# Kernel optimization log

Measured on AMD Instinct MI355X. Metric: run time of the kernel, lower is better.

Reference implementation:

```python
import jax, jax.numpy as jnp
import numpy as np

N_QUBITS = 4
N_LAYERS = 2
FS = 2          # filter_size
STRIDE = 1
DIM = 2 ** N_QUBITS  # 16

# mean over qubits of PauliZ eigenvalue per computational-basis state
_idx = np.arange(DIM)
_bits = np.stack([(_idx >> (N_QUBITS - 1 - q)) & 1 for q in range(N_QUBITS)], 0)  # [4,16]
Z_MEAN = jnp.asarray((1.0 - 2.0 * _bits).mean(0), dtype=jnp.float32)               # [16]


def ry_mat(t):
    c, s = jnp.cos(t / 2), jnp.sin(t / 2)
    m = jnp.stack([jnp.stack([c, -s], -1), jnp.stack([s, c], -1)], -2)
    return m.astype(jnp.complex64)


def rx_mat(t):
    c = jnp.cos(t / 2).astype(jnp.complex64)
    s = (jnp.sin(t / 2) * (-1j)).astype(jnp.complex64)
    return jnp.stack([jnp.stack([c, s], -1), jnp.stack([s, c], -1)], -2)


def rz_mat(t):
    e = jnp.exp((t / 2).astype(jnp.complex64) * (-1j))
    z = jnp.zeros_like(e)
    return jnp.stack([jnp.stack([e, z], -1), jnp.stack([z, jnp.conj(e)], -1)], -2)


def apply_1q(state, U, q):
    # state: [N,2,2,2,2] complex; U: [2,2] or batched [N,2,2]
    st = jnp.moveaxis(state, 1 + q, -1)
    if U.ndim == 3:
        st = jnp.einsum('nab,n...b->n...a', U, st)
    else:
        st = jnp.einsum('ab,n...b->n...a', U, st)
    return jnp.moveaxis(st, -1, 1 + q)


def apply_cnot(state, c, t):
    st = jnp.moveaxis(state, (1 + c, 1 + t), (-2, -1))
    st = jnp.stack([st[..., 0, :], st[..., 1, ::-1]], axis=-2)
    return jnp.moveaxis(st, (-2, -1), (1 + c, 1 + t))


def apply_cry(state, theta, c, t):
    U = ry_mat(theta)
    st = jnp.moveaxis(state, (1 + c, 1 + t), (-2, -1))
    bot = jnp.einsum('ab,n...b->n...a', U, st[..., 1, :])
    st = jnp.stack([st[..., 0, :], bot], axis=-2)
    return jnp.moveaxis(st, (-2, -1), (1 + c, 1 + t))


def _forward(x, weights):
    B, H, W, C = x.shape
    oh = (H - FS) // STRIDE + 1
    ow = (W - FS) // STRIDE + 1
    # extract all patches at once: [B, oh, ow, FS, FS, C]
    ri = (jnp.arange(oh) * STRIDE)[:, None, None, None] + jnp.arange(FS)[None, None, :, None]
    ci = (jnp.arange(ow) * STRIDE)[None, :, None, None] + jnp.arange(FS)[None, None, None, :]
    patches = x[:, ri, ci, :]
    pf = patches.reshape(B * oh * ow, FS * FS * C)
    # tf.nn.l2_normalize over the whole (flat) patch, eps=1e-12
    norm = pf * jax.lax.rsqrt(jnp.maximum(jnp.sum(pf * pf, -1, keepdims=True), 1e-12))
    ang = norm[:, :N_QUBITS]  # RY angles, [N,4]
    N = pf.shape[0]

    # |0000> encoded state, batched over all patches
    state = jnp.zeros((N, DIM), jnp.complex64).at[:, 0].set(1.0)
    state = state.reshape((N,) + (2,) * N_QUBITS)
    for q in range(N_QUBITS):
        state = apply_1q(state, ry_mat(ang[:, q]), q)
    for q in range(N_QUBITS - 1):
        state = apply_cnot(state, q, q + 1)

    outs = []
    for f in range(weights.shape[0]):
        w = weights[f]
        s = state
        for layer in range(N_LAYERS):
            base = layer * N_QUBITS * 3
            for q in range(N_QUBITS):
                p = base + q * 3
                s = apply_1q(s, rx_mat(w[p]), q)
                s = apply_1q(s, ry_mat(w[p + 1]), q)
                s = apply_1q(s, rz_mat(w[p + 2]), q)
            # CRY on even pairs, reusing weights[base + i] (as in the source)
            for q in range(0, N_QUBITS - 1, 2):
                s = apply_cry(s, w[base + q], q, q + 1)
        sf = s.reshape(N, DIM)
        probs = jnp.real(sf * jnp.conj(sf))           # [N,16]
        outs.append((probs @ Z_MEAN).reshape(B, oh, ow))  # mean of <Z_q>
    return jnp.stack(outs, -1)  # [B, oh, ow, n_filters]


def setup_inputs() -> dict:
    key = jax.random.key(0)
    k1, k2 = jax.random.split(key)
    x = jax.random.normal(k1, (8, 96, 96, 16), dtype=jnp.float32)
    # keras 'random_uniform' initializer default range
    weights = jax.random.uniform(k2, (8, 24), dtype=jnp.float32, minval=-0.05, maxval=0.05)
    return {"x": x, "weights": weights}


def reference(x, weights):
    return _forward(x, weights)
```

## Files before the change

### kernel.cpp

```cpp
#include <hip/hip_runtime.h>

namespace {
constexpr int DIM = 16;
constexpr int BATCH = 8;
constexpr int H = 96, W = 96, CH = 16;
constexpr int OH = 95, OW = 95;
constexpr int NF = 8, NW = 24;
constexpr int NPIX = BATCH * OH * OW;
constexpr int PSIBLK = (NPIX + 255) / 256;
constexpr int PSI_OFF = NF * 256;
constexpr int PPB = 128;
constexpr int ABLK = (NPIX + PPB - 1) / PPB;
}

__device__ __forceinline__ int permf(int i) {
  int j = i;
  if (j & 8) j ^= 4;
  if (j & 4) j ^= 2;
  if (j & 2) j ^= 1;
  return j;
}

__global__ __launch_bounds__(256)
void prep_kernel(const float* __restrict__ x, const float* __restrict__ wts,
                 float* __restrict__ ws) {
  const int tid = threadIdx.x;
  if (blockIdx.x == PSIBLK) {
    __shared__ float ur[NF * 256];
    __shared__ float ui[NF * 256];
    const int f = tid >> 4;
    const int col = tid & 15;
    if (tid < NF * DIM) {
      const float* w = wts + f * NW;
      float ar[DIM], ai[DIM];
#pragma unroll
      for (int i = 0; i < DIM; ++i) { ar[i] = (i == col) ? 1.f : 0.f; ai[i] = 0.f; }
#pragma unroll
      for (int layer = 0; layer < 2; ++layer) {
        const int wb = layer * 12;
#pragma unroll
        for (int q = 0; q < 4; ++q) {
          const int m = 8 >> q;
          float c, s;
          {
            __sincosf(w[wb + q * 3] * 0.5f, &s, &c);
#pragma unroll
            for (int i = 0; i < DIM; ++i) {
              if (i & m) continue;
              const int j = i | m;
              const float a0r = ar[i], a0i = ai[i], a1r = ar[j], a1i = ai[j];
              ar[i] = fmaf(c, a0r,  s * a1i);
              ai[i] = fmaf(c, a0i, -s * a1r);
              ar[j] = fmaf(c, a1r,  s * a0i);
              ai[j] = fmaf(c, a1i, -s * a0r);
            }
          }
          {
            __sincosf(w[wb + q * 3 + 1] * 0.5f, &s, &c);
#pragma unroll
            for (int i = 0; i < DIM; ++i) {
              if (i & m) continue;
              const int j = i | m;
              const float a0r = ar[i], a0i = ai[i], a1r = ar[j], a1i = ai[j];
              ar[i] = fmaf(c, a0r, -s * a1r);
              ai[i] = fmaf(c, a0i, -s * a1i);
              ar[j] = fmaf(s, a0r,  c * a1r);
              ai[j] = fmaf(s, a0i,  c * a1i);
            }
          }
          {
            __sincosf(w[wb + q * 3 + 2] * 0.5f, &s, &c);
#pragma unroll
            for (int i = 0; i < DIM; ++i) {
              const float r = ar[i], im = ai[i];
              if (i & m) { ar[i] = fmaf(c, r, -s * im); ai[i] = fmaf(c, im,  s * r); }
              else       { ar[i] = fmaf(c, r,  s * im); ai[i] = fmaf(c, im, -s * r); }
            }
          }
        }
        {
          float c, s;
          __sincosf(w[wb + 0] * 0.5f, &s, &c);
#pragma unroll
          for (int i = 0; i < DIM; ++i) {
            if (!(i & 8) || (i & 4)) continue;
            const int j = i | 4;
            const float a0r = ar[i], a0i = ai[i], a1r = ar[j], a1i = ai[j];
            ar[i] = fmaf(c, a0r, -s * a1r);
            ai[i] = fmaf(c, a0i, -s * a1i);
            ar[j] = fmaf(s, a0r,  c * a1r);
            ai[j] = fmaf(s, a0i,  c * a1i);
          }
        }
        {
          float c, s;
          __sincosf(w[wb + 2] * 0.5f, &s, &c);
#pragma unroll
          for (int i = 0; i < DIM; ++i) {
            if (!(i & 2) || (i & 1)) continue;
            const int j = i | 1;
            const float a0r = ar[i], a0i = ai[i], a1r = ar[j], a1i = ai[j];
            ar[i] = fmaf(c, a0r, -s * a1r);
            ai[i] = fmaf(c, a0i, -s * a1i);
            ar[j] = fmaf(s, a0r,  c * a1r);
            ai[j] = fmaf(s, a0i,  c * a1i);
          }
        }
      }
#pragma unroll
      for (int i = 0; i < DIM; ++i) {
        ur[f * 256 + col * 16 + i] = ar[i];
        ui[f * 256 + col * 16 + i] = ai[i];
      }
    }
    __syncthreads();
    if (tid < NF * DIM) {
      const int k = col;
      const int pk = permf(k);
      const float* cr = ur + f * 256;
      const float* ci = ui + f * 256;
      float* dst = ws + f * 256 + k * 16;
#pragma unroll
      for (int j = 0; j < DIM; ++j) {
        const int pj = permf(j);
        float acc = 0.f;
#pragma unroll
        for (int i = 0; i < DIM; ++i) {
          const float z = 1.f - 0.5f * (float)__popc(i);
          acc += z * (cr[pk * 16 + i] * cr[pj * 16 + i] +
                      ci[pk * 16 + i] * ci[pj * 16 + i]);
        }
        dst[j] = acc;
      }
    }
  } else {
    const int n = blockIdx.x * 256 + tid;
    if (n >= NPIX) return;
    const int b = n / (OH * OW);
    const int rem = n - b * (OH * OW);
    const int oi = rem / OW;
    const int oj = rem - oi * OW;

    const float* base = x + (((b * H) + oi) * W + oj) * CH;
    float ss = 0.f;
    float4 f0 = make_float4(0.f, 0.f, 0.f, 0.f);
#pragma unroll
    for (int fi = 0; fi < 2; ++fi) {
      const float4* row = reinterpret_cast<const float4*>(base + fi * W * CH);
#pragma unroll
      for (int k = 0; k < 8; ++k) {
        const float4 v = row[k];
        if (fi == 0 && k == 0) f0 = v;
        ss = fmaf(v.x, v.x, ss); ss = fmaf(v.y, v.y, ss);
        ss = fmaf(v.z, v.z, ss); ss = fmaf(v.w, v.w, ss);
      }
    }
    const float inv = rsqrtf(fmaxf(ss, 1e-12f));

    float cq[4], sq[4];
    __sincosf(f0.x * inv * 0.5f, &sq[0], &cq[0]);
    __sincosf(f0.y * inv * 0.5f, &sq[1], &cq[1]);
    __sincosf(f0.z * inv * 0.5f, &sq[2], &cq[2]);
    __sincosf(f0.w * inv * 0.5f, &sq[3], &cq[3]);

    float st[DIM];
#pragma unroll
    for (int i = 0; i < DIM; ++i) {
      st[i] = ((i & 8) ? sq[0] : cq[0]) * ((i & 4) ? sq[1] : cq[1]) *
              ((i & 2) ? sq[2] : cq[2]) * ((i & 1) ? sq[3] : cq[3]);
    }
    float4* dst = reinterpret_cast<float4*>(ws + PSI_OFF + n * 16);
    dst[0] = make_float4(st[0], st[1], st[2], st[3]);
    dst[1] = make_float4(st[4], st[5], st[6], st[7]);
    dst[2] = make_float4(st[8], st[9], st[10], st[11]);
    dst[3] = make_float4(st[12], st[13], st[14], st[15]);
  }
}

__global__ __launch_bounds__(512)
void apply_kernel(const float* __restrict__ ws, float* __restrict__ out) {
  __shared__ float os[PPB * 9];
  const int tid = threadIdx.x;
  const int lane = tid & 63;
  const int f = __builtin_amdgcn_readfirstlane(tid >> 6);
  const float* __restrict__ M = ws + f * 256;
  const int pbase = blockIdx.x * PPB;

  const int n0 = pbase + lane;
  const int n1 = pbase + 64 + lane;
  const int c0 = n0 < NPIX ? n0 : NPIX - 1;
  const int c1 = n1 < NPIX ? n1 : NPIX - 1;

  float pa[DIM], pb[DIM];
  {
    const float4* p0 = reinterpret_cast<const float4*>(ws + PSI_OFF + c0 * 16);
    const float4 a0 = p0[0], a1 = p0[1], a2 = p0[2], a3 = p0[3];
    pa[0] = a0.x;  pa[1] = a0.y;  pa[2] = a0.z;  pa[3] = a0.w;
    pa[4] = a1.x;  pa[5] = a1.y;  pa[6] = a1.z;  pa[7] = a1.w;
    pa[8] = a2.x;  pa[9] = a2.y;  pa[10] = a2.z; pa[11] = a2.w;
    pa[12] = a3.x; pa[13] = a3.y; pa[14] = a3.z; pa[15] = a3.w;
    const float4* p1 = reinterpret_cast<const float4*>(ws + PSI_OFF + c1 * 16);
    const float4 b0 = p1[0], b1 = p1[1], b2 = p1[2], b3 = p1[3];
    pb[0] = b0.x;  pb[1] = b0.y;  pb[2] = b0.z;  pb[3] = b0.w;
    pb[4] = b1.x;  pb[5] = b1.y;  pb[6] = b1.z;  pb[7] = b1.w;
    pb[8] = b2.x;  pb[9] = b2.y;  pb[10] = b2.z; pb[11] = b2.w;
    pb[12] = b3.x; pb[13] = b3.y; pb[14] = b3.z; pb[15] = b3.w;
  }

  float ya[DIM], yb[DIM];
#pragma unroll
  for (int i = 0; i < DIM; ++i) { ya[i] = 0.f; yb[i] = 0.f; }

#pragma unroll
  for (int k = 0; k < DIM; ++k) {
    const float ak = pa[k];
    const float bk = pb[k];
#pragma unroll
    for (int j = 0; j < DIM; ++j) {
      const float m = M[k * 16 + j];
      ya[j] = fmaf(m, ak, ya[j]);
      yb[j] = fmaf(m, bk, yb[j]);
    }
  }

  float a0 = 0.f, a1 = 0.f, a2 = 0.f, a3 = 0.f;
  float b0 = 0.f, b1 = 0.f, b2 = 0.f, b3 = 0.f;
#pragma unroll
  for (int i = 0; i < DIM; i += 4) {
    a0 = fmaf(pa[i + 0], ya[i + 0], a0);
    a1 = fmaf(pa[i + 1], ya[i + 1], a1);
    a2 = fmaf(pa[i + 2], ya[i + 2], a2);
    a3 = fmaf(pa[i + 3], ya[i + 3], a3);
    b0 = fmaf(pb[i + 0], yb[i + 0], b0);
    b1 = fmaf(pb[i + 1], yb[i + 1], b1);
    b2 = fmaf(pb[i + 2], yb[i + 2], b2);
    b3 = fmaf(pb[i + 3], yb[i + 3], b3);
  }
  os[lane * 9 + f] = (a0 + a1) + (a2 + a3);
  os[(64 + lane) * 9 + f] = (b0 + b1) + (b2 + b3);
  __syncthreads();

  const int j2 = tid * 2;
  const int p = j2 >> 3;
  const int e = j2 & 7;
  const long gi = (long)pbase * 8 + j2;
  if (gi + 1 < (long)NPIX * 8) {
    const float v0 = os[p * 9 + e];
    const float v1 = os[p * 9 + e + 1];
    *reinterpret_cast<float2*>(out + gi) = make_float2(v0, v1);
  }
}

extern "C" void kernel_launch(void* const* d_in, const int* in_sizes, int n_in,
                              void* d_out, int out_size, void* d_ws, size_t ws_size,
                              hipStream_t stream) {
  const float* x = (const float*)d_in[0];
  const float* w = (const float*)d_in[1];
  float* out = (float*)d_out;
  float* ws = (float*)d_ws;

  prep_kernel<<<dim3(PSIBLK + 1), dim3(256), 0, stream>>>(x, w, ws);
  apply_kernel<<<dim3(ABLK), dim3(512), 0, stream>>>(ws, out);
}
```

Measured before the change: 76.60 us.

## Fuse psi construction into apply kernel and split M build into own kernel

The per-pixel product-state construction moves out of the prep kernel and into the apply kernel, which now builds the psi vectors in shared memory. This removes the global round trip of 16 floats per pixel through the workspace. The M-matrix build becomes a separate small kernel with one block per filter, and the apply kernel stages all eight M matrices in LDS and reads them as float4. In exchange, only 128 of 512 threads do the patch loads and norm, so there is a serial phase with low thread utilization before the barrier.

```diff
diff --git a/kernel.cpp b/kernel.cpp
--- a/kernel.cpp
+++ b/kernel.cpp
@@ -7,8 +7,6 @@
 constexpr int OH = 95, OW = 95;
 constexpr int NF = 8, NW = 24;
 constexpr int NPIX = BATCH * OH * OW;
-constexpr int PSIBLK = (NPIX + 255) / 256;
-constexpr int PSI_OFF = NF * 256;
 constexpr int PPB = 128;
 constexpr int ABLK = (NPIX + PPB - 1) / PPB;
 }
@@ -22,69 +20,44 @@
 }
 
 __global__ __launch_bounds__(256)
-void prep_kernel(const float* __restrict__ x, const float* __restrict__ wts,
-                 float* __restrict__ ws) {
+void build_m_kernel(const float* __restrict__ wts, float* __restrict__ ws) {
+  __shared__ float ur[DIM * 17];
+  __shared__ float ui[DIM * 17];
+  const int f = blockIdx.x;
   const int tid = threadIdx.x;
-  if (blockIdx.x == PSIBLK) {
-    __shared__ float ur[NF * 256];
-    __shared__ float ui[NF * 256];
-    const int f = tid >> 4;
-    const int col = tid & 15;
-    if (tid < NF * DIM) {
-      const float* w = wts + f * NW;
-      float ar[DIM], ai[DIM];
-#pragma unroll
-      for (int i = 0; i < DIM; ++i) { ar[i] = (i == col) ? 1.f : 0.f; ai[i] = 0.f; }
-#pragma unroll
-      for (int layer = 0; layer < 2; ++layer) {
-        const int wb = layer * 12;
-#pragma unroll
-        for (int q = 0; q < 4; ++q) {
-          const int m = 8 >> q;
-          float c, s;
-          {
-            __sincosf(w[wb + q * 3] * 0.5f, &s, &c);
-#pragma unroll
-            for (int i = 0; i < DIM; ++i) {
-              if (i & m) continue;
-              const int j = i | m;
-              const float a0r = ar[i], a0i = ai[i], a1r = ar[j], a1i = ai[j];
-              ar[i] = fmaf(c, a0r,  s * a1i);
-              ai[i] = fmaf(c, a0i, -s * a1r);
-              ar[j] = fmaf(c, a1r,  s * a0i);
-              ai[j] = fmaf(c, a1i, -s * a0r);
-            }
+
+  if (tid < DIM) {
+    const int col = tid;
+    const float* w = wts + f * NW;
+    float ar[DIM], ai[DIM];
+#pragma unroll
+    for (int i = 0; i < DIM; ++i) { ar[i] = (i == col) ? 1.f : 0.f; ai[i] = 0.f; }
+#pragma unroll
+    for (int layer = 0; layer < 2; ++layer) {
+      const int wb = layer * 12;
+#pragma unroll
+      for (int q = 0; q < 4; ++q) {
+        const int m = 8 >> q;
+        float c, s;
+        {
+          __sincosf(w[wb + q * 3] * 0.5f, &s, &c);
+#pragma unroll
+          for (int i = 0; i < DIM; ++i) {
+            if (i & m) continue;
+            const int j = i | m;
+            const float a0r = ar[i], a0i = ai[i], a1r = ar[j], a1i = ai[j];
+            ar[i] = fmaf(c, a0r,  s * a1i);
+            ai[i] = fmaf(c, a0i, -s * a1r);
+            ar[j] = fmaf(c, a1r,  s * a0i);
+            ai[j] = fmaf(c, a1i, -s * a0r);
           }
-          {
-            __sincosf(w[wb + q * 3 + 1] * 0.5f, &s, &c);
-#pragma unroll
-            for (int i = 0; i < DIM; ++i) {
-              if (i & m) continue;
-              const int j = i | m;
-              const float a0r = ar[i], a0i = ai[i], a1r = ar[j], a1i = ai[j];
-              ar[i] = fmaf(c, a0r, -s * a1r);
-              ai[i] = fmaf(c, a0i, -s * a1i);
-              ar[j] = fmaf(s, a0r,  c * a1r);
-              ai[j] = fmaf(s, a0i,  c * a1i);
-            }
-          }
-          {
-            __sincosf(w[wb + q * 3 + 2] * 0.5f, &s, &c);
-#pragma unroll
-            for (int i = 0; i < DIM; ++i) {
-              const float r = ar[i], im = ai[i];
-              if (i & m) { ar[i] = fmaf(c, r, -s * im); ai[i] = fmaf(c, im,  s * r); }
-              else       { ar[i] = fmaf(c, r,  s * im); ai[i] = fmaf(c, im, -s * r); }
-            }
-          }
         }
         {
-          float c, s;
-          __sincosf(w[wb + 0] * 0.5f, &s, &c);
+          __sincosf(w[wb + q * 3 + 1] * 0.5f, &s, &c);
 #pragma unroll
           for (int i = 0; i < DIM; ++i) {
-            if (!(i & 8) || (i & 4)) continue;
-            const int j = i | 4;
+            if (i & m) continue;
+            const int j = i | m;
             const float a0r = ar[i], a0i = ai[i], a1r = ar[j], a1i = ai[j];
             ar[i] = fmaf(c, a0r, -s * a1r);
             ai[i] = fmaf(c, a0i, -s * a1i);
@@ -93,49 +66,78 @@
           }
         }
         {
-          float c, s;
-          __sincosf(w[wb + 2] * 0.5f, &s, &c);
+          __sincosf(w[wb + q * 3 + 2] * 0.5f, &s, &c);
 #pragma unroll
           for (int i = 0; i < DIM; ++i) {
-            if (!(i & 2) || (i & 1)) continue;
-            const int j = i | 1;
-            const float a0r = ar[i], a0i = ai[i], a1r = ar[j], a1i = ai[j];
-            ar[i] = fmaf(c, a0r, -s * a1r);
-            ai[i] = fmaf(c, a0i, -s * a1i);
-            ar[j] = fmaf(s, a0r,  c * a1r);
-            ai[j] = fmaf(s, a0i,  c * a1i);
+            const float r = ar[i], im = ai[i];
+            if (i & m) { ar[i] = fmaf(c, r, -s * im); ai[i] = fmaf(c, im,  s * r); }
+            else       { ar[i] = fmaf(c, r,  s * im); ai[i] = fmaf(c, im, -s * r); }
           }
         }
       }
-#pragma unroll
-      for (int i = 0; i < DIM; ++i) {
-        ur[f * 256 + col * 16 + i] = ar[i];
-        ui[f * 256 + col * 16 + i] = ai[i];
-      }
-    }
-    __syncthreads();
-    if (tid < NF * DIM) {
-      const int k = col;
-      const int pk = permf(k);
-      const float* cr = ur + f * 256;
-      const float* ci = ui + f * 256;
-      float* dst = ws + f * 256 + k * 16;
-#pragma unroll
-      for (int j = 0; j < DIM; ++j) {
-        const int pj = permf(j);
-        float acc = 0.f;
+      {
+        float c, s;
+        __sincosf(w[wb + 0] * 0.5f, &s, &c);
 #pragma unroll
         for (int i = 0; i < DIM; ++i) {
-          const float z = 1.f - 0.5f * (float)__popc(i);
-          acc += z * (cr[pk * 16 + i] * cr[pj * 16 + i] +
-                      ci[pk * 16 + i] * ci[pj * 16 + i]);
-        }
-        dst[j] = acc;
-      }
-    }
-  } else {
-    const int n = blockIdx.x * 256 + tid;
-    if (n >= NPIX) return;
+          if (!(i & 8) || (i & 4)) continue;
+          const int j = i | 4;
+          const float a0r = ar[i], a0i = ai[i], a1r = ar[j], a1i = ai[j];
+          ar[i] = fmaf(c, a0r, -s * a1r);
+          ai[i] = fmaf(c, a0i, -s * a1i);
+          ar[j] = fmaf(s, a0r,  c * a1r);
+          ai[j] = fmaf(s, a0i,  c * a1i);
+        }
+      }
+      {
+        float c, s;
+        __sincosf(w[wb + 2] * 0.5f, &s, &c);
+#pragma unroll
+        for (int i = 0; i < DIM; ++i) {
+          if (!(i & 2) || (i & 1)) continue;
+          const int j = i | 1;
+          const float a0r = ar[i], a0i = ai[i], a1r = ar[j], a1i = ai[j];
+          ar[i] = fmaf(c, a0r, -s * a1r);
+          ai[i] = fmaf(c, a0i, -s * a1i);
+          ar[j] = fmaf(s, a0r,  c * a1r);
+          ai[j] = fmaf(s, a0i,  c * a1i);
+        }
+      }
+    }
+#pragma unroll
+    for (int i = 0; i < DIM; ++i) {
+      ur[i * 17 + col] = ar[i];
+      ui[i * 17 + col] = ai[i];
+    }
+  }
+  __syncthreads();
+
+  const int k = tid >> 4;
+  const int j = tid & 15;
+  const int pk = permf(k);
+  const int pj = permf(j);
+  float acc = 0.f;
+#pragma unroll
+  for (int i = 0; i < DIM; ++i) {
+    const float z = 1.f - 0.5f * (float)__popc(i);
+    acc = fmaf(z * ur[i * 17 + pk], ur[i * 17 + pj], acc);
+    acc = fmaf(z * ui[i * 17 + pk], ui[i * 17 + pj], acc);
+  }
+  ws[f * 256 + k * 16 + j] = acc;
+}
+
+__global__ __launch_bounds__(512)
+void fused_kernel(const float* __restrict__ x, const float* __restrict__ ws,
+                  float* __restrict__ out) {
+  __shared__ float Ml[NF * 256];
+  __shared__ float psis[PPB * 17];
+  __shared__ float os[PPB * 9];
+  const int tid = threadIdx.x;
+  const int pbase = blockIdx.x * PPB;
+
+  if (tid < PPB) {
+    int n = pbase + tid;
+    if (n >= NPIX) n = NPIX - 1;
     const int b = n / (OH * OW);
     const int rem = n - b * (OH * OW);
     const int oi = rem / OW;
@@ -163,48 +165,29 @@
     __sincosf(f0.z * inv * 0.5f, &sq[2], &cq[2]);
     __sincosf(f0.w * inv * 0.5f, &sq[3], &cq[3]);
 
-    float st[DIM];
 #pragma unroll
     for (int i = 0; i < DIM; ++i) {
-      st[i] = ((i & 8) ? sq[0] : cq[0]) * ((i & 4) ? sq[1] : cq[1]) *
-              ((i & 2) ? sq[2] : cq[2]) * ((i & 1) ? sq[3] : cq[3]);
-    }
-    float4* dst = reinterpret_cast<float4*>(ws + PSI_OFF + n * 16);
-    dst[0] = make_float4(st[0], st[1], st[2], st[3]);
-    dst[1] = make_float4(st[4], st[5], st[6], st[7]);
-    dst[2] = make_float4(st[8], st[9], st[10], st[11]);
-    dst[3] = make_float4(st[12], st[13], st[14], st[15]);
-  }
-}
-
-__global__ __launch_bounds__(512)
-void apply_kernel(const float* __restrict__ ws, float* __restrict__ out) {
-  __shared__ float os[PPB * 9];
-  const int tid = threadIdx.x;
+      psis[tid * 17 + i] =
+          ((i & 8) ? sq[0] : cq[0]) * ((i & 4) ? sq[1] : cq[1]) *
+          ((i & 2) ? sq[2] : cq[2]) * ((i & 1) ? sq[3] : cq[3]);
+    }
+  } else if (tid < 384) {
+    const int i = tid - 128;
+    const float4* src = reinterpret_cast<const float4*>(ws);
+    reinterpret_cast<float4*>(Ml)[i] = src[i];
+    reinterpret_cast<float4*>(Ml)[i + 256] = src[i + 256];
+  }
+  __syncthreads();
+
   const int lane = tid & 63;
   const int f = __builtin_amdgcn_readfirstlane(tid >> 6);
-  const float* __restrict__ M = ws + f * 256;
-  const int pbase = blockIdx.x * PPB;
-
-  const int n0 = pbase + lane;
-  const int n1 = pbase + 64 + lane;
-  const int c0 = n0 < NPIX ? n0 : NPIX - 1;
-  const int c1 = n1 < NPIX ? n1 : NPIX - 1;
+  const float* Mrow = Ml + f * 256;
 
   float pa[DIM], pb[DIM];
-  {
-    const float4* p0 = reinterpret_cast<const float4*>(ws + PSI_OFF + c0 * 16);
-    const float4 a0 = p0[0], a1 = p0[1], a2 = p0[2], a3 = p0[3];
-    pa[0] = a0.x;  pa[1] = a0.y;  pa[2] = a0.z;  pa[3] = a0.w;
-    pa[4] = a1.x;  pa[5] = a1.y;  pa[6] = a1.z;  pa[7] = a1.w;
-    pa[8] = a2.x;  pa[9] = a2.y;  pa[10] = a2.z; pa[11] = a2.w;
-    pa[12] = a3.x; pa[13] = a3.y; pa[14] = a3.z; pa[15] = a3.w;
-    const float4* p1 = reinterpret_cast<const float4*>(ws + PSI_OFF + c1 * 16);
-    const float4 b0 = p1[0], b1 = p1[1], b2 = p1[2], b3 = p1[3];
-    pb[0] = b0.x;  pb[1] = b0.y;  pb[2] = b0.z;  pb[3] = b0.w;
-    pb[4] = b1.x;  pb[5] = b1.y;  pb[6] = b1.z;  pb[7] = b1.w;
-    pb[8] = b2.x;  pb[9] = b2.y;  pb[10] = b2.z; pb[11] = b2.w;
-    pb[12] = b3.x; pb[13] = b3.y; pb[14] = b3.z; pb[15] = b3.w;
+#pragma unroll
+  for (int k = 0; k < DIM; ++k) {
+    pa[k] = psis[lane * 17 + k];
+    pb[k] = psis[(64 + lane) * 17 + k];
   }
 
   float ya[DIM], yb[DIM];
@@ -215,12 +198,26 @@
   for (int k = 0; k < DIM; ++k) {
     const float ak = pa[k];
     const float bk = pb[k];
-#pragma unroll
-    for (int j = 0; j < DIM; ++j) {
-      const float m = M[k * 16 + j];
-      ya[j] = fmaf(m, ak, ya[j]);
-      yb[j] = fmaf(m, bk, yb[j]);
-    }
+    const float4 m0 = *reinterpret_cast<const float4*>(Mrow + k * 16 + 0);
+    const float4 m1 = *reinterpret_cast<const float4*>(Mrow + k * 16 + 4);
+    const float4 m2 = *reinterpret_cast<const float4*>(Mrow + k * 16 + 8);
+    const float4 m3 = *reinterpret_cast<const float4*>(Mrow + k * 16 + 12);
+    ya[0]  = fmaf(m0.x, ak, ya[0]);  yb[0]  = fmaf(m0.x, bk, yb[0]);
+    ya[1]  = fmaf(m0.y, ak, ya[1]);  yb[1]  = fmaf(m0.y, bk, yb[1]);
+    ya[2]  = fmaf(m0.z, ak, ya[2]);  yb[2]  = fmaf(m0.z, bk, yb[2]);
+    ya[3]  = fmaf(m0.w, ak, ya[3]);  yb[3]  = fmaf(m0.w, bk, yb[3]);
+    ya[4]  = fmaf(m1.x, ak, ya[4]);  yb[4]  = fmaf(m1.x, bk, yb[4]);
+    ya[5]  = fmaf(m1.y, ak, ya[5]);  yb[5]  = fmaf(m1.y, bk, yb[5]);
+    ya[6]  = fmaf(m1.z, ak, ya[6]);  yb[6]  = fmaf(m1.z, bk, yb[6]);
+    ya[7]  = fmaf(m1.w, ak, ya[7]);  yb[7]  = fmaf(m1.w, bk, yb[7]);
+    ya[8]  = fmaf(m2.x, ak, ya[8]);  yb[8]  = fmaf(m2.x, bk, yb[8]);
+    ya[9]  = fmaf(m2.y, ak, ya[9]);  yb[9]  = fmaf(m2.y, bk, yb[9]);
+    ya[10] = fmaf(m2.z, ak, ya[10]); yb[10] = fmaf(m2.z, bk, yb[10]);
+    ya[11] = fmaf(m2.w, ak, ya[11]); yb[11] = fmaf(m2.w, bk, yb[11]);
+    ya[12] = fmaf(m3.x, ak, ya[12]); yb[12] = fmaf(m3.x, bk, yb[12]);
+    ya[13] = fmaf(m3.y, ak, ya[13]); yb[13] = fmaf(m3.y, bk, yb[13]);
+    ya[14] = fmaf(m3.z, ak, ya[14]); yb[14] = fmaf(m3.z, bk, yb[14]);
+    ya[15] = fmaf(m3.w, ak, ya[15]); yb[15] = fmaf(m3.w, bk, yb[15]);
   }
 
   float a0 = 0.f, a1 = 0.f, a2 = 0.f, a3 = 0.f;
@@ -245,9 +242,8 @@
   const int e = j2 & 7;
   const long gi = (long)pbase * 8 + j2;
   if (gi + 1 < (long)NPIX * 8) {
-    const float v0 = os[p * 9 + e];
-    const float v1 = os[p * 9 + e + 1];
-    *reinterpret_cast<float2*>(out + gi) = make_float2(v0, v1);
+    *reinterpret_cast<float2*>(out + gi) =
+        make_float2(os[p * 9 + e], os[p * 9 + e + 1]);
   }
 }
 
@@ -259,6 +255,6 @@
   float* out = (float*)d_out;
   float* ws = (float*)d_ws;
 
-  prep_kernel<<<dim3(PSIBLK + 1), dim3(256), 0, stream>>>(x, w, ws);
-  apply_kernel<<<dim3(ABLK), dim3(512), 0, stream>>>(ws, out);
-}
+  build_m_kernel<<<dim3(NF), dim3(256), 0, stream>>>(w, ws);
+  fused_kernel<<<dim3(ABLK), dim3(512), 0, stream>>>(x, ws, out);
+}
```

New measurement: 69.28 us. 1.11x faster.
